# Kernel tuning notes

Measured on AMD Instinct MI355X. Metric: run time of the kernel, lower is better.

The kernel has to match this reference:

```python
import jax, jax.numpy as jnp
import numpy as np

POOLING_RATIO = 0.5  # matches init kwarg
N_NODES = 16384
N_EDGES = 524288
D_FEAT = 128


def setup_inputs() -> dict:
    key = jax.random.key(0)
    k1, k2, k3, k4 = jax.random.split(key, 4)
    return {
        "pos": jax.random.normal(k1, (N_NODES, 3), jnp.float32),
        "feat": jax.random.normal(k2, (N_NODES, D_FEAT), jnp.float32),
        "src": jax.random.randint(k3, (N_EDGES,), 0, N_NODES, jnp.int32),
        "dst": jax.random.randint(k4, (N_EDGES,), 0, N_NODES, jnp.int32),
        "batch_size": 4,
    }


def _fps(p, k):
    # Farthest point sampling on one cloud p: [n, 3]. Deterministic start at idx 0
    # (DGL uses a random start; we fix it for reproducibility).
    n = p.shape[0]
    def step(carry, _):
        dists, last = carry  # dists: min sq-dist to selected set so far
        d = jnp.sum((p - p[last]) ** 2, axis=-1)
        dists = jnp.minimum(dists, d)
        nxt = jnp.argmax(dists).astype(jnp.int32)
        return (dists, nxt), last
    init = (jnp.full((n,), 1e10, p.dtype), jnp.asarray(0, jnp.int32))
    _, idx = jax.lax.scan(step, init, None, length=k)
    return idx  # [k]


def reference(pos, feat, src, dst, batch_size):
    N = pos.shape[0]
    n_points = N // batch_size
    k = round(n_points * (1.0 - POOLING_RATIO))  # downsampled points per cloud

    # ---- farthest point sampling per cloud ----
    p = pos.reshape(batch_size, n_points, pos.shape[-1])  # [B, n, 3]
    fp = jax.vmap(lambda q: _fps(q, k))(p)                # [B, k] local ids
    offs = (jnp.arange(batch_size, dtype=jnp.int32) * n_points)[:, None]
    fp_idx = (fp + offs).reshape(-1)                      # [B*k] global ids

    # ---- copy_u + mean aggregation on the FULL graph (G.update_all) ----
    deg = jax.ops.segment_sum(jnp.ones_like(dst, dtype=feat.dtype), dst, num_segments=N)
    agg = jax.ops.segment_sum(feat[src], dst, num_segments=N)  # [N, D]
    agg = agg / jnp.maximum(deg, 1.0)[:, None]  # nodes with no in-edges stay 0

    # ---- induced subgraph gather ----
    M = fp_idx.shape[0]
    sub_x = pos[fp_idx]      # [M, 3]
    sub_feat = agg[fp_idx]   # [M, D]

    # induced subgraph edges: keep original edges whose endpoints are both sampled
    inv = jnp.full((N,), -1, jnp.int32).at[fp_idx].set(jnp.arange(M, dtype=jnp.int32))
    ls, ld = inv[src], inv[dst]
    edge_mask = (ls >= 0) & (ld >= 0)
    ls = jnp.where(edge_mask, ls, 0)
    ld = jnp.where(edge_mask, ld, 0)

    # per-edge displacement and norm on subgraph positions
    d = jnp.where(edge_mask[:, None], sub_x[ld] - sub_x[ls], 0.0)  # [E, 3]
    w = jnp.sqrt(jnp.sum(d ** 2, axis=-1, keepdims=True))          # [E, 1]

    return sub_x, sub_feat, d, w, edge_mask, fp_idx
```

## Files before the change

kernel.cpp:

```cpp
#include <hip/hip_runtime.h>
#include <math.h>

#define N_NODES 16384
#define N_EDGES 524288
#define D_FEAT  128
#define BATCH   4
#define NPTS    4096
#define KSEL    2048
#define MSEL    (BATCH*KSEL)

#define X16(F) F(0) F(1) F(2) F(3) F(4) F(5) F(6) F(7) \
               F(8) F(9) F(10) F(11) F(12) F(13) F(14) F(15)


__device__ __forceinline__ unsigned long long dpp_max_step(unsigned long long p,
                                                           unsigned int slo,
                                                           unsigned int shi)
{
    unsigned long long s = (((unsigned long long)shi) << 32) | slo;
    return (s > p) ? s : p;
}

__launch_bounds__(256, 1)
__global__ void fps_kernel(const float* __restrict__ pos,
                           int* __restrict__ fp_int,
                           int* __restrict__ inv,
                           float* __restrict__ out_subx,
                           float* __restrict__ out_fp)
{
    __shared__ float sx[NPTS];
    __shared__ float sy[NPTS];
    __shared__ float sz[NPTS];
    __shared__ int   sel[KSEL];
    __shared__ unsigned long long pwv[2][4];

    const int b   = blockIdx.x;
    const int tid = threadIdx.x;

    const float* gp = pos + (size_t)b * NPTS * 3;
    for (int i = tid; i < NPTS; i += 256) {
        sx[i] = gp[3 * i + 0];
        sy[i] = gp[3 * i + 1];
        sz[i] = gp[3 * i + 2];
    }
    __syncthreads();

#define DECL(J) float x##J, y##J, z##J, d##J;
    X16(DECL)
#undef DECL
#define LOAD(J) { int li = (J)*256 + tid; x##J = sx[li]; y##J = sy[li]; z##J = sz[li]; d##J = 1e10f; }
    X16(LOAD)
#undef LOAD

    int cur = 0;
    for (int t = 0; t < KSEL; ++t) {
        if (tid == 0) sel[t] = cur;
        float qx = sx[cur];
        float qy = sy[cur];
        float qz = sz[cur];

        float bv = -1.0f;
        int   bi = 0x7fffffff;
#define UPD(J) { \
        float dx = __fsub_rn(x##J, qx); \
        float dy = __fsub_rn(y##J, qy); \
        float dz = __fsub_rn(z##J, qz); \
        float dd = __fadd_rn(__fadd_rn(__fmul_rn(dx, dx), __fmul_rn(dy, dy)), \
                             __fmul_rn(dz, dz)); \
        d##J = fminf(d##J, dd); \
        if (d##J > bv) { bv = d##J; bi = (J)*256 + tid; } }
        X16(UPD)
#undef UPD

        unsigned long long p =
            (((unsigned long long)__float_as_uint(bv)) << 32) |
            (unsigned int)(~bi);

        {
            unsigned int lo, hi, slo, shi;
#define DSTEP(CTRL) \
            lo = (unsigned int)p; hi = (unsigned int)(p >> 32); \
            slo = __builtin_amdgcn_update_dpp(0, (int)lo, CTRL, 0xf, 0xf, true); \
            shi = __builtin_amdgcn_update_dpp(0, (int)hi, CTRL, 0xf, 0xf, true); \
            p = dpp_max_step(p, slo, shi);
            DSTEP(0x111)
            DSTEP(0x112)
            DSTEP(0x114)
            DSTEP(0x118)
            DSTEP(0x142)
            DSTEP(0x143)
#undef DSTEP
        }

        int par = t & 1;
        if ((tid & 63) == 63) pwv[par][tid >> 6] = p;
        __syncthreads();

        unsigned long long c0 = pwv[par][0];
        unsigned long long c1 = pwv[par][1];
        unsigned long long c2 = pwv[par][2];
        unsigned long long c3 = pwv[par][3];
        unsigned long long m01 = (c0 > c1) ? c0 : c1;
        unsigned long long m23 = (c2 > c3) ? c2 : c3;
        unsigned long long mm  = (m01 > m23) ? m01 : m23;
        cur = (int)(~(unsigned int)(mm & 0xffffffffULL));
    }
    __syncthreads();

    for (int t = tid; t < KSEL; t += 256) {
        int c = sel[t];
        int g = b * NPTS + c;
        int m = b * KSEL + t;
        fp_int[m] = g;
        inv[g] = m;
        out_fp[m] = (float)g;
        out_subx[m * 3 + 0] = sx[c];
        out_subx[m * 3 + 1] = sy[c];
        out_subx[m * 3 + 2] = sz[c];
    }
}

__global__ void deg_kernel(const int* __restrict__ dst, int* __restrict__ deg,
                           int* __restrict__ inv)
{
    int e = blockIdx.x * blockDim.x + threadIdx.x;
    if (e < N_NODES) inv[e] = -1;
    if (e < N_EDGES) atomicAdd(&deg[dst[e]], 1);
}

__global__ void scan_kernel(const int* __restrict__ deg, int* __restrict__ row_ptr,
                            int* __restrict__ row_ptr2)
{
    __shared__ int part[1024];
    int tid = threadIdx.x;
    int base = tid * 16;
    int local[16];
    int s = 0;
#pragma unroll
    for (int j = 0; j < 16; ++j) { local[j] = s; s += deg[base + j]; }
    part[tid] = s;
    __syncthreads();
    for (int off = 1; off < 1024; off <<= 1) {
        int v = part[tid];
        int add = (tid >= off) ? part[tid - off] : 0;
        __syncthreads();
        part[tid] = v + add;
        __syncthreads();
    }
    int prefix = (tid == 0) ? 0 : part[tid - 1];
#pragma unroll
    for (int j = 0; j < 16; ++j) {
        int v = prefix + local[j];
        row_ptr[base + j]  = v;
        row_ptr2[base + j] = v;
    }
    if (tid == 1023) row_ptr[N_NODES] = part[1023];
}

__global__ void scatter_kernel(const int* __restrict__ src, const int* __restrict__ dst,
                               int* __restrict__ row_ptr2, int* __restrict__ col)
{
    int e = blockIdx.x * blockDim.x + threadIdx.x;
    if (e < N_EDGES) {
        int r = atomicAdd(&row_ptr2[dst[e]], 1);
        col[r] = src[e];
    }
}

__global__ void agg_edge_kernel(const float* __restrict__ feat,
                                const int* __restrict__ fp_int,
                                const int* __restrict__ row_ptr,
                                const int* __restrict__ col,
                                const int* __restrict__ deg,
                                float* __restrict__ out_subfeat,
                                const int* __restrict__ src,
                                const int* __restrict__ dst,
                                const int* __restrict__ inv,
                                const float* __restrict__ subx,
                                float* __restrict__ outd,
                                float* __restrict__ outw,
                                float* __restrict__ outm)
{
    if (blockIdx.x < 2048) {
        int wid  = (blockIdx.x * blockDim.x + threadIdx.x) >> 6;
        int lane = threadIdx.x & 63;
        int v  = fp_int[wid];
        int s0 = row_ptr[v];
        int s1 = row_ptr[v + 1];
        float a0 = 0.0f, a1 = 0.0f, b0 = 0.0f, b1 = 0.0f;
        int e = s0;
        for (; e + 1 < s1; e += 2) {
            int sA = col[e];
            int sB = col[e + 1];
            float2 vA = ((const float2*)(feat + (size_t)sA * D_FEAT))[lane];
            float2 vB = ((const float2*)(feat + (size_t)sB * D_FEAT))[lane];
            a0 += vA.x; a1 += vA.y;
            b0 += vB.x; b1 += vB.y;
        }
        if (e < s1) {
            int sA = col[e];
            float2 vA = ((const float2*)(feat + (size_t)sA * D_FEAT))[lane];
            a0 += vA.x; a1 += vA.y;
        }
        a0 += b0; a1 += b1;
        float dv = fmaxf((float)deg[v], 1.0f);
        float* o = out_subfeat + (size_t)wid * D_FEAT + lane * 2;
        o[0] = a0 / dv;
        o[1] = a1 / dv;
    } else {
        int e = (blockIdx.x - 2048) * blockDim.x + threadIdx.x;
        int ls = inv[src[e]];
        int ld = inv[dst[e]];
        bool mk = (ls >= 0) && (ld >= 0);
        float dx = 0.0f, dy = 0.0f, dz = 0.0f;
        if (mk) {
            dx = __fsub_rn(subx[ld * 3 + 0], subx[ls * 3 + 0]);
            dy = __fsub_rn(subx[ld * 3 + 1], subx[ls * 3 + 1]);
            dz = __fsub_rn(subx[ld * 3 + 2], subx[ls * 3 + 2]);
        }
        float w = sqrtf(__fadd_rn(__fadd_rn(__fmul_rn(dx, dx), __fmul_rn(dy, dy)),
                                  __fmul_rn(dz, dz)));
        outd[e * 3 + 0] = dx;
        outd[e * 3 + 1] = dy;
        outd[e * 3 + 2] = dz;
        outw[e] = w;
        outm[e] = mk ? 1.0f : 0.0f;
    }
}

extern "C" void kernel_launch(void* const* d_in, const int* in_sizes, int n_in,
                              void* d_out, int out_size, void* d_ws, size_t ws_size,
                              hipStream_t stream)
{
    const float* pos  = (const float*)d_in[0];
    const float* feat = (const float*)d_in[1];
    const int*   src  = (const int*)d_in[2];
    const int*   dst  = (const int*)d_in[3];

    float* out = (float*)d_out;
    float* out_subx    = out;
    float* out_subfeat = out_subx + (size_t)MSEL * 3;
    float* out_d       = out_subfeat + (size_t)MSEL * D_FEAT;
    float* out_w       = out_d + (size_t)N_EDGES * 3;
    float* out_m       = out_w + (size_t)N_EDGES;
    float* out_fp      = out_m + (size_t)N_EDGES;

    int* fp_int   = (int*)d_ws;
    int* inv      = fp_int + MSEL;
    int* deg      = inv + N_NODES;
    int* row_ptr  = deg + N_NODES;
    int* row_ptr2 = row_ptr + (N_NODES + 1);
    int* col      = row_ptr2 + (N_NODES + 1);

    (void)hipMemsetAsync(deg, 0, (size_t)N_NODES * 4, stream);

    deg_kernel<<<N_EDGES / 256, 256, 0, stream>>>(dst, deg, inv);
    scan_kernel<<<1, 1024, 0, stream>>>(deg, row_ptr, row_ptr2);
    scatter_kernel<<<N_EDGES / 256, 256, 0, stream>>>(src, dst, row_ptr2, col);

    fps_kernel<<<BATCH, 256, 0, stream>>>(pos, fp_int, inv, out_subx, out_fp);

    agg_edge_kernel<<<4096, 256, 0, stream>>>(feat, fp_int, row_ptr, col, deg,
                                              out_subfeat, src, dst, inv, out_subx,
                                              out_d, out_w, out_m);
}
```

Before: 1.261 ms.

## Spatially sort points into Morton chunks and skip unaffected chunks in FPS

The FPS kernel now bins each cloud's points into an 8x8x8 Morton grid, sorts them into shared memory, and splits them into 32 chunks of 128 points, each with a bounding box and a cached per-chunk maximum. At every iteration only chunks whose box lower bound could lower their current maximum are recomputed; the others keep their cached candidate. This is meant to avoid updating all 4096 distances per step in the serial 2048-step loop, at the cost of setup work, more shared-memory traffic, and wave-level load imbalance when few chunks are dirty. Ties break on original index to match the argmax order.

```diff
diff --git a/kernel.cpp b/kernel.cpp
--- a/kernel.cpp
+++ b/kernel.cpp
@@ -8,9 +8,8 @@
 #define NPTS    4096
 #define KSEL    2048
 #define MSEL    (BATCH*KSEL)
-
-#define X16(F) F(0) F(1) F(2) F(3) F(4) F(5) F(6) F(7) \
-               F(8) F(9) F(10) F(11) F(12) F(13) F(14) F(15)
+#define NCHUNK  32
+#define CH_SH   7
 
 
 __device__ __forceinline__ unsigned long long dpp_max_step(unsigned long long p,
@@ -19,6 +18,41 @@
 {
     unsigned long long s = (((unsigned long long)shi) << 32) | slo;
     return (s > p) ? s : p;
+}
+
+__device__ __forceinline__ unsigned long long wave_max_u64(unsigned long long p)
+{
+    unsigned int lo, hi, slo, shi;
+#define DSTEP(CTRL) \
+    lo = (unsigned int)p; hi = (unsigned int)(p >> 32); \
+    slo = __builtin_amdgcn_update_dpp(0, (int)lo, CTRL, 0xf, 0xf, true); \
+    shi = __builtin_amdgcn_update_dpp(0, (int)hi, CTRL, 0xf, 0xf, true); \
+    p = dpp_max_step(p, slo, shi);
+    DSTEP(0x111) DSTEP(0x112) DSTEP(0x114) DSTEP(0x118) DSTEP(0x142) DSTEP(0x143)
+#undef DSTEP
+    return p;
+}
+
+__device__ __forceinline__ float wave_min_f32(float v)
+{
+#define MSTEP(CTRL) { int r_ = __builtin_amdgcn_update_dpp(__float_as_int(v), \
+        __float_as_int(v), CTRL, 0xf, 0xf, false); v = fminf(v, __int_as_float(r_)); }
+    MSTEP(0x111) MSTEP(0x112) MSTEP(0x114) MSTEP(0x118) MSTEP(0x142) MSTEP(0x143)
+#undef MSTEP
+    return v;
+}
+__device__ __forceinline__ float wave_max_f32(float v)
+{
+#define MSTEP(CTRL) { int r_ = __builtin_amdgcn_update_dpp(__float_as_int(v), \
+        __float_as_int(v), CTRL, 0xf, 0xf, false); v = fmaxf(v, __int_as_float(r_)); }
+    MSTEP(0x111) MSTEP(0x112) MSTEP(0x114) MSTEP(0x118) MSTEP(0x142) MSTEP(0x143)
+#undef MSTEP
+    return v;
+}
+
+__device__ __forceinline__ int spread3(int c)
+{
+    return (c & 1) | ((c & 2) << 2) | ((c & 4) << 4);
 }
 
 __launch_bounds__(256, 1)
@@ -28,95 +62,196 @@
                            float* __restrict__ out_subx,
                            float* __restrict__ out_fp)
 {
-    __shared__ float sx[NPTS];
-    __shared__ float sy[NPTS];
-    __shared__ float sz[NPTS];
-    __shared__ int   sel[KSEL];
-    __shared__ unsigned long long pwv[2][4];
-
-    const int b   = blockIdx.x;
-    const int tid = threadIdx.x;
-
+    __shared__ float ssx[NPTS], ssy[NPTS], ssz[NPTS];
+    __shared__ float sdist[NPTS];
+    __shared__ int   sperm[NPTS];
+    __shared__ int   sel_o[KSEL], sel_s[KSEL];
+    __shared__ float bbl[3][NCHUNK], bbh[3][NCHUNK];
+    __shared__ unsigned cand_hi[2][NCHUNK], cand_lo[2][NCHUNK];
+    __shared__ int   hist[512];
+    __shared__ int   part[256];
+    __shared__ float cb[8];
+    __shared__ int   s0pos;
+
+    const int b    = blockIdx.x;
+    const int tid  = threadIdx.x;
+    const int lane = tid & 63;
+    const int wv   = tid >> 6;
     const float* gp = pos + (size_t)b * NPTS * 3;
+
+    {
+        float mnx = 1e30f, mny = 1e30f, mnz = 1e30f;
+        float mxx = -1e30f, mxy = -1e30f, mxz = -1e30f;
+        for (int i = tid; i < NPTS; i += 256) {
+            float x = gp[3*i+0], y = gp[3*i+1], z = gp[3*i+2];
+            mnx = fminf(mnx, x); mny = fminf(mny, y); mnz = fminf(mnz, z);
+            mxx = fmaxf(mxx, x); mxy = fmaxf(mxy, y); mxz = fmaxf(mxz, z);
+        }
+        sdist[tid]        = mnx; sdist[256 + tid]  = mny; sdist[512 + tid]  = mnz;
+        sdist[768 + tid]  = mxx; sdist[1024 + tid] = mxy; sdist[1280 + tid] = mxz;
+        hist[tid]       = 0;
+        hist[tid + 256] = 0;
+        __syncthreads();
+        if (tid < 6) {
+            int base = tid * 256;
+            float v = sdist[base];
+            for (int i = 1; i < 256; ++i) {
+                float u = sdist[base + i];
+                v = (tid < 3) ? fminf(v, u) : fmaxf(v, u);
+            }
+            cb[tid] = v;
+        }
+        __syncthreads();
+    }
+    float lox = cb[0], loy = cb[1], loz = cb[2];
+    float ex = cb[3] - lox, ey = cb[4] - loy, ez = cb[5] - loz;
+    float scx = (ex > 0.0f) ? 7.999f / ex : 0.0f;
+    float scy = (ey > 0.0f) ? 7.999f / ey : 0.0f;
+    float scz = (ez > 0.0f) ? 7.999f / ez : 0.0f;
+
     for (int i = tid; i < NPTS; i += 256) {
-        sx[i] = gp[3 * i + 0];
-        sy[i] = gp[3 * i + 1];
-        sz[i] = gp[3 * i + 2];
+        float x = gp[3*i+0], y = gp[3*i+1], z = gp[3*i+2];
+        int cx = min(7, max(0, (int)((x - lox) * scx)));
+        int cy = min(7, max(0, (int)((y - loy) * scy)));
+        int cz = min(7, max(0, (int)((z - loz) * scz)));
+        int code = (spread3(cx) << 2) | (spread3(cy) << 1) | spread3(cz);
+        atomicAdd(&hist[code], 1);
     }
     __syncthreads();
-
-#define DECL(J) float x##J, y##J, z##J, d##J;
-    X16(DECL)
-#undef DECL
-#define LOAD(J) { int li = (J)*256 + tid; x##J = sx[li]; y##J = sy[li]; z##J = sz[li]; d##J = 1e10f; }
-    X16(LOAD)
-#undef LOAD
-
-    int cur = 0;
+    {
+        int h0 = hist[2*tid], h1 = hist[2*tid+1];
+        part[tid] = h0 + h1;
+        __syncthreads();
+        for (int off = 1; off < 256; off <<= 1) {
+            int v = part[tid];
+            int a = (tid >= off) ? part[tid - off] : 0;
+            __syncthreads();
+            part[tid] = v + a;
+            __syncthreads();
+        }
+        int excl = (tid == 0) ? 0 : part[tid - 1];
+        hist[2*tid]   = excl;
+        hist[2*tid+1] = excl + h0;
+        __syncthreads();
+    }
+    for (int i = tid; i < NPTS; i += 256) {
+        float x = gp[3*i+0], y = gp[3*i+1], z = gp[3*i+2];
+        int cx = min(7, max(0, (int)((x - lox) * scx)));
+        int cy = min(7, max(0, (int)((y - loy) * scy)));
+        int cz = min(7, max(0, (int)((z - loz) * scz)));
+        int code = (spread3(cx) << 2) | (spread3(cy) << 1) | spread3(cz);
+        int p = atomicAdd(&hist[code], 1);
+        ssx[p] = x; ssy[p] = y; ssz[p] = z; sperm[p] = i;
+        if (i == 0) s0pos = p;
+    }
+    __syncthreads();
+    for (int c = wv; c < NCHUNK; c += 4) {
+        int j0 = (c << CH_SH) + lane, j1 = j0 + 64;
+        float ax = ssx[j0], bx = ssx[j1];
+        float ay = ssy[j0], by = ssy[j1];
+        float az = ssz[j0], bz = ssz[j1];
+        float mnx = wave_min_f32(fminf(ax, bx));
+        float mxx = wave_max_f32(fmaxf(ax, bx));
+        float mny = wave_min_f32(fminf(ay, by));
+        float mxy = wave_max_f32(fmaxf(ay, by));
+        float mnz = wave_min_f32(fminf(az, bz));
+        float mxz = wave_max_f32(fmaxf(az, bz));
+        if (lane == 63) {
+            bbl[0][c] = mnx; bbh[0][c] = mxx;
+            bbl[1][c] = mny; bbh[1][c] = mxy;
+            bbl[2][c] = mnz; bbh[2][c] = mxz;
+        }
+    }
+    for (int i = tid; i < NPTS; i += 256) sdist[i] = 1e10f;
+    if (tid < NCHUNK) {
+        cand_hi[1][tid] = 0x7F800000u;
+        cand_lo[1][tid] = 0u;
+    }
+    __syncthreads();
+
+    int cur_orig = 0;
+    int cur_sorted = s0pos;
+    float qx = ssx[cur_sorted], qy = ssy[cur_sorted], qz = ssz[cur_sorted];
+
     for (int t = 0; t < KSEL; ++t) {
-        if (tid == 0) sel[t] = cur;
-        float qx = sx[cur];
-        float qy = sy[cur];
-        float qz = sz[cur];
-
-        float bv = -1.0f;
-        int   bi = 0x7fffffff;
-#define UPD(J) { \
-        float dx = __fsub_rn(x##J, qx); \
-        float dy = __fsub_rn(y##J, qy); \
-        float dz = __fsub_rn(z##J, qz); \
-        float dd = __fadd_rn(__fadd_rn(__fmul_rn(dx, dx), __fmul_rn(dy, dy)), \
-                             __fmul_rn(dz, dz)); \
-        d##J = fminf(d##J, dd); \
-        if (d##J > bv) { bv = d##J; bi = (J)*256 + tid; } }
-        X16(UPD)
-#undef UPD
-
-        unsigned long long p =
-            (((unsigned long long)__float_as_uint(bv)) << 32) |
-            (unsigned int)(~bi);
+        if (tid == 0) { sel_o[t] = cur_orig; sel_s[t] = cur_sorted; }
+        int par = t & 1;
+
+        int c0 = lane & 31;
+        float ux = fmaxf(0.0f, fmaxf(bbl[0][c0] - qx, qx - bbh[0][c0]));
+        float uy = fmaxf(0.0f, fmaxf(bbl[1][c0] - qy, qy - bbh[1][c0]));
+        float uz = fmaxf(0.0f, fmaxf(bbl[2][c0] - qz, qz - bbh[2][c0]));
+        float bnd = __fadd_rn(__fadd_rn(__fmul_rn(ux,ux), __fmul_rn(uy,uy)),
+                              __fmul_rn(uz,uz)) * 0.99999f;
+        float cmax = __int_as_float((int)cand_hi[par ^ 1][c0]);
+        bool dirty = (lane < 32) && !(bnd > cmax);
+        unsigned m32 = (unsigned)__ballot(dirty);
+
+        if (lane < 32 && !((m32 >> lane) & 1)) {
+            cand_hi[par][lane] = cand_hi[par ^ 1][lane];
+            cand_lo[par][lane] = cand_lo[par ^ 1][lane];
+        }
 
         {
-            unsigned int lo, hi, slo, shi;
-#define DSTEP(CTRL) \
-            lo = (unsigned int)p; hi = (unsigned int)(p >> 32); \
-            slo = __builtin_amdgcn_update_dpp(0, (int)lo, CTRL, 0xf, 0xf, true); \
-            shi = __builtin_amdgcn_update_dpp(0, (int)hi, CTRL, 0xf, 0xf, true); \
-            p = dpp_max_step(p, slo, shi);
-            DSTEP(0x111)
-            DSTEP(0x112)
-            DSTEP(0x114)
-            DSTEP(0x118)
-            DSTEP(0x142)
-            DSTEP(0x143)
-#undef DSTEP
-        }
-
-        int par = t & 1;
-        if ((tid & 63) == 63) pwv[par][tid >> 6] = p;
-        __syncthreads();
-
-        unsigned long long c0 = pwv[par][0];
-        unsigned long long c1 = pwv[par][1];
-        unsigned long long c2 = pwv[par][2];
-        unsigned long long c3 = pwv[par][3];
-        unsigned long long m01 = (c0 > c1) ? c0 : c1;
-        unsigned long long m23 = (c2 > c3) ? c2 : c3;
-        unsigned long long mm  = (m01 > m23) ? m01 : m23;
-        cur = (int)(~(unsigned int)(mm & 0xffffffffULL));
+            unsigned m = m32; int r = 0;
+            while (m) {
+                int c = __ffs(m) - 1; m &= m - 1;
+                if ((r & 3) == wv) {
+                    int j0 = (c << CH_SH) + lane, j1 = j0 + 64;
+                    float ax = ssx[j0], ay = ssy[j0], az = ssz[j0];
+                    float bx = ssx[j1], by = ssy[j1], bz = ssz[j1];
+                    float d0 = sdist[j0], d1 = sdist[j1];
+                    int   o0 = sperm[j0], o1 = sperm[j1];
+                    float dx0 = __fsub_rn(ax, qx), dy0 = __fsub_rn(ay, qy), dz0 = __fsub_rn(az, qz);
+                    float dd0 = __fadd_rn(__fadd_rn(__fmul_rn(dx0,dx0), __fmul_rn(dy0,dy0)),
+                                          __fmul_rn(dz0,dz0));
+                    float dx1 = __fsub_rn(bx, qx), dy1 = __fsub_rn(by, qy), dz1 = __fsub_rn(bz, qz);
+                    float dd1 = __fadd_rn(__fadd_rn(__fmul_rn(dx1,dx1), __fmul_rn(dy1,dy1)),
+                                          __fmul_rn(dz1,dz1));
+                    float n0 = fminf(d0, dd0); sdist[j0] = n0;
+                    float n1 = fminf(d1, dd1); sdist[j1] = n1;
+                    unsigned long long p0 =
+                        (((unsigned long long)__float_as_uint(n0)) << 32) |
+                        (((unsigned)(4095 - o0)) << 20) | (((unsigned)j0) << 8);
+                    unsigned long long p1 =
+                        (((unsigned long long)__float_as_uint(n1)) << 32) |
+                        (((unsigned)(4095 - o1)) << 20) | (((unsigned)j1) << 8);
+                    unsigned long long p = (p1 > p0) ? p1 : p0;
+                    p = wave_max_u64(p);
+                    if (lane == 63) {
+                        cand_hi[par][c] = (unsigned)(p >> 32);
+                        cand_lo[par][c] = (unsigned)p;
+                    }
+                }
+                ++r;
+            }
+        }
+
+        __syncthreads();
+
+        {
+            unsigned chi = cand_hi[par][c0];
+            unsigned clo = cand_lo[par][c0];
+            unsigned long long p = (((unsigned long long)chi) << 32) | clo;
+            p = wave_max_u64(p);
+            unsigned wlo = (unsigned)__builtin_amdgcn_readlane((int)(unsigned)p, 63);
+            cur_sorted = (int)((wlo >> 8) & 0xFFFu);
+            cur_orig   = 4095 - (int)((wlo >> 20) & 0xFFFu);
+            qx = ssx[cur_sorted]; qy = ssy[cur_sorted]; qz = ssz[cur_sorted];
+        }
     }
     __syncthreads();
 
     for (int t = tid; t < KSEL; t += 256) {
-        int c = sel[t];
-        int g = b * NPTS + c;
-        int m = b * KSEL + t;
+        int so = sel_s[t];
+        int g  = b * NPTS + sel_o[t];
+        int m  = b * KSEL + t;
         fp_int[m] = g;
         inv[g] = m;
         out_fp[m] = (float)g;
-        out_subx[m * 3 + 0] = sx[c];
-        out_subx[m * 3 + 1] = sy[c];
-        out_subx[m * 3 + 2] = sz[c];
+        out_subx[m * 3 + 0] = ssx[so];
+        out_subx[m * 3 + 1] = ssy[so];
+        out_subx[m * 3 + 2] = ssz[so];
     }
 }
 
```

New measurement: 2.645 ms. 110% more time.
